# Performance work log

Measured on AMD Instinct MI355X. Metric: run time of the kernel, lower is better.

## Reference

```python
import jax, jax.numpy as jnp
import numpy as np
from jax.scipy.special import logsumexp

B, F, V, C, K, KP = 8192, 32, 64, 32, 8, 7  # batch, features, values/feature, classes, gate options, padded pair candidates
TEMP = 1.0
EPS = 1e-06


def _structure():
    # candidate 0 = self table; candidates 1..7 = pair tables conditioned on preceding features
    mask = np.zeros((F - 1, K), dtype=bool)
    mask[:, 0] = True
    cond = np.zeros((F - 1, KP), dtype=np.int32)
    for i in range(F - 1):
        fi = i + 1
        for j in range(min(fi, KP)):
            mask[i, j + 1] = True
            cond[i, j] = fi - 1 - j
    return jnp.asarray(cond), jnp.asarray(mask)


def setup_inputs() -> dict:
    key = jax.random.key(0)
    ks = jax.random.split(key, 6)
    cond_index, valid_mask = _structure()
    return {
        "x": jax.random.randint(ks[0], (B, F), 0, V, dtype=jnp.int32),
        "training": True,
        "class_logits": jax.random.normal(ks[1], (C,), jnp.float32) * 0.1,
        "table0": jax.random.normal(ks[2], (V, C), jnp.float32) * 0.1,
        "self_tables": jax.random.normal(ks[3], (F - 1, V, C), jnp.float32) * 0.1,
        "pair_tables": jax.random.normal(ks[4], (F - 1, KP, V, V, C), jnp.float32) * 0.1,
        "structure_logits": jax.random.normal(ks[5], (F - 1, K), jnp.float32) * 0.1,
        "u_noise": jax.random.uniform(jax.random.fold_in(key, 7), (F - 1, K), jnp.float32),
        "cond_index": cond_index,
        "valid_mask": valid_mask,
    }


def reference(x, training, class_logits, table0, self_tables, pair_tables,
              structure_logits, u_noise, cond_index, valid_mask):
    # class prior term
    cl = class_logits - logsumexp(class_logits)  # [C]
    t0 = table0 - logsumexp(table0, axis=0, keepdims=True)  # [V,C]
    out = cl[None, :] + t0[x[:, 0]]  # [B,C]

    # Gumbel-softmax gate over candidate parent sets (training path)
    g = -jnp.log(-jnp.log(u_noise + EPS) + EPS)
    gate_logits = jnp.where(valid_mask, (structure_logits + g) / TEMP, -jnp.inf)
    w = jax.nn.softmax(gate_logits, axis=-1)  # [F-1,K]; padded entries get weight 0

    f_idx = jnp.arange(F - 1)
    xs = x[:, 1:]  # [B,F-1] feature values

    # self (class-only) candidate tables, normalized over the feature-value axis
    st = self_tables - logsumexp(self_tables, axis=1, keepdims=True)  # [F-1,V,C]
    self_g = st[f_idx[None, :], xs]  # [B,F-1,C]
    out = out + jnp.einsum('bfc,f->bc', self_g, w[:, 0])

    # pair candidate tables, normalized over the feature-value axis (axis 2)
    pt = pair_tables - logsumexp(pair_tables, axis=2, keepdims=True)  # [F-1,KP,V,V,C]
    xc = x[:, cond_index]  # [B,F-1,KP] conditioning feature values
    k_idx = jnp.arange(KP)
    pair_g = pt[f_idx[None, :, None], k_idx[None, None, :], xs[:, :, None], xc]  # [B,F-1,KP,C]
    out = out + jnp.einsum('bfkc,fk->bc', pair_g, w[:, 1:])
    return out
```

## Files before the change

kernel.cpp:

```cpp
#include <hip/hip_runtime.h>
#include <math.h>

#define B_  8192
#define F_  32
#define V_  64
#define C_  32
#define KP_ 7
#define EPS_ 1e-6f

#define WS_G 512

__global__ __launch_bounds__(1024)
void prep_kernel(const float* __restrict__ cl, const float* __restrict__ t0,
                 const float* __restrict__ st, const float* __restrict__ sl,
                 const float* __restrict__ un, float* __restrict__ ws) {
    __shared__ float gl[31][8];
    __shared__ float wsm[31][8];
    __shared__ float lse_self[31][32];
    int tid = threadIdx.x;

    if (tid < 248) {
        int f = tid >> 3, k = tid & 7;
        int kmax = min(f + 1, KP_);
        bool valid = (k <= kmax);
        float u = un[tid];
        float g = -__logf(-__logf(u + EPS_) + EPS_);
        gl[f][k] = valid ? (sl[tid] + g) : -INFINITY;
    }
    __syncthreads();
    if (tid < 248) {
        int f = tid >> 3, k = tid & 7;
        float m = -INFINITY;
        #pragma unroll
        for (int j = 0; j < 8; j++) m = fmaxf(m, gl[f][j]);
        float s = 0.f;
        #pragma unroll
        for (int j = 0; j < 8; j++) s += __expf(gl[f][j] - m);
        float wv = __expf(gl[f][k] - m) / s;
        wsm[f][k] = wv;
        ws[tid] = wv;
    }
    if (tid < 992) {
        int f = tid >> 5, c = tid & 31;
        float s = 0.f;
        #pragma unroll 8
        for (int v = 0; v < V_; v++) s += __expf(st[(f * V_ + v) * C_ + c]);
        lse_self[f][c] = __logf(s);
    }
    __syncthreads();
    if (tid < 32) {
        int c = tid;
        float scl = 0.f;
        #pragma unroll
        for (int j = 0; j < C_; j++) scl += __expf(cl[j]);
        float lse_cl = __logf(scl);
        float s0 = 0.f;
        #pragma unroll 8
        for (int v = 0; v < V_; v++) s0 += __expf(t0[v * C_ + c]);
        float lse_t0 = __logf(s0);
        float acc = cl[c] - lse_cl - lse_t0;
        for (int f = 0; f < 31; f++) acc -= wsm[f][0] * lse_self[f][c];
        ws[256 + c] = acc;
    }
}

__global__ __launch_bounds__(256)
void build_g_kernel(const float* __restrict__ t0, const float* __restrict__ st,
                    const float* __restrict__ pt, const float* __restrict__ ws,
                    float* __restrict__ G) {
    int idx = blockIdx.x * 256 + threadIdx.x;
    int c = idx & 31, v = (idx >> 5) & 63, j = idx >> 11;
    int nk = min(KP_, 31 - j);
    const float* bp[KP_];
    #pragma unroll
    for (int k = 0; k < KP_; k++) {
        int f = j + k;
        int fk = f * KP_ + k;
        bp[k] = pt + (fk * (V_ * V_) + v) * C_ + c;
    }
    float s[KP_];
    #pragma unroll
    for (int k = 0; k < KP_; k++) s[k] = 0.f;
    for (int a = 0; a < V_; a += 2) {
        float l0[KP_], l1[KP_];
        #pragma unroll
        for (int k = 0; k < KP_; k++) if (k < nk) {
            l0[k] = bp[k][a * (V_ * C_)];
            l1[k] = bp[k][(a + 1) * (V_ * C_)];
        }
        #pragma unroll
        for (int k = 0; k < KP_; k++) if (k < nk) {
            s[k] += __expf(l0[k]);
            s[k] += __expf(l1[k]);
        }
    }
    float g = 0.f;
    #pragma unroll
    for (int k = 0; k < KP_; k++) if (k < nk)
        g -= ws[(j + k) * 8 + k + 1] * __logf(s[k]);
    if (j == 0) g += t0[v * C_ + c];
    else        g += ws[(j - 1) * 8] * st[((j - 1) * V_ + v) * C_ + c];
    G[idx] = g;
}

__global__ __launch_bounds__(256)
void main_kernel(const int* __restrict__ x, const float* __restrict__ pt,
                 const float* __restrict__ ws, float* __restrict__ out) {
    __shared__ int   xsh[256];
    __shared__ float wsh[248];
    __shared__ float offsh[32];
    int tid = threadIdx.x;
    int fchunk = blockIdx.x >> 10;
    int bblk   = blockIdx.x & 1023;
    xsh[tid] = x[bblk * 256 + tid];
    if (tid < 248) wsh[tid] = ws[tid];
    if (tid < 32)  offsh[tid] = ws[256 + tid];
    __syncthreads();

    const float* __restrict__ G = ws + WS_G;
    int c = tid & 31;
    int r = tid >> 5;
    const int* xrow = &xsh[r * 32];
    float acc = 0.f;

    if (fchunk == 0) {
        acc = offsh[c];
        #pragma unroll
        for (int j = 0; j < 16; j++)
            acc += G[(j * V_ + xrow[j]) * C_ + c];
        for (int f = 0; f < 6; f++) {
            int xv = xrow[f + 1];
            const float* bp = pt + ((f * KP_) * V_ + xv) * (V_ * C_) + c;
            float pv[6];
            for (int k = 0; k <= f; k++)
                pv[k] = bp[k * (V_ * V_ * C_) + xrow[f - k] * C_];
            for (int k = 0; k <= f; k++)
                acc += wsh[f * 8 + k + 1] * pv[k];
        }
        #pragma unroll 2
        for (int f = 6; f < 17; f++) {
            int xv = xrow[f + 1];
            const float* bp = pt + ((f * KP_) * V_ + xv) * (V_ * C_) + c;
            float pv[KP_];
            #pragma unroll
            for (int k = 0; k < KP_; k++)
                pv[k] = bp[k * (V_ * V_ * C_) + xrow[f - k] * C_];
            #pragma unroll
            for (int k = 0; k < KP_; k++)
                acc += wsh[f * 8 + k + 1] * pv[k];
        }
    } else {
        #pragma unroll
        for (int j = 16; j < 32; j++)
            acc += G[(j * V_ + xrow[j]) * C_ + c];
        #pragma unroll 2
        for (int f = 17; f < 31; f++) {
            int xv = xrow[f + 1];
            const float* bp = pt + ((f * KP_) * V_ + xv) * (V_ * C_) + c;
            float pv[KP_];
            #pragma unroll
            for (int k = 0; k < KP_; k++)
                pv[k] = bp[k * (V_ * V_ * C_) + xrow[f - k] * C_];
            #pragma unroll
            for (int k = 0; k < KP_; k++)
                acc += wsh[f * 8 + k + 1] * pv[k];
        }
    }
    atomicAdd(&out[bblk * 256 + tid], acc);
}

extern "C" void kernel_launch(void* const* d_in, const int* in_sizes, int n_in,
                              void* d_out, int out_size, void* d_ws, size_t ws_size,
                              hipStream_t stream) {
    const int*   x   = (const int*)  d_in[0];
    const float* cl  = (const float*)d_in[2];
    const float* t0  = (const float*)d_in[3];
    const float* st  = (const float*)d_in[4];
    const float* pt  = (const float*)d_in[5];
    const float* sl  = (const float*)d_in[6];
    const float* un  = (const float*)d_in[7];
    float* ws  = (float*)d_ws;
    float* out = (float*)d_out;

    hipMemsetAsync(out, 0, (size_t)B_ * C_ * sizeof(float), stream);
    prep_kernel<<<1, 1024, 0, stream>>>(cl, t0, st, sl, un, ws);
    build_g_kernel<<<256, 256, 0, stream>>>(t0, st, pt, ws, ws + WS_G);
    main_kernel<<<2048, 256, 0, stream>>>(x, pt, ws, out);
}
```

Measured before the change: 233.5 us.

## Split features across warps within a block and reduce in shared memory instead of atomics

Each block now covers two batch rows instead of eight. Its four 64-thread groups each take a balanced slice of the G-table lookups and pair-table gathers, roughly 49 pair gathers per group. Partial sums are combined through shared memory and written once with a plain store. This removes the output memset and the global atomicAdds, and doubles the number of blocks to give more parallelism. In exchange it adds a block-wide barrier and leaves three quarters of the threads idle during the final store.

```diff
diff --git a/kernel.cpp b/kernel.cpp
--- a/kernel.cpp
+++ b/kernel.cpp
@@ -106,28 +106,31 @@
 __global__ __launch_bounds__(256)
 void main_kernel(const int* __restrict__ x, const float* __restrict__ pt,
                  const float* __restrict__ ws, float* __restrict__ out) {
-    __shared__ int   xsh[256];
+    __shared__ int   xsh[64];
     __shared__ float wsh[248];
     __shared__ float offsh[32];
+    __shared__ float part[3][64];
     int tid = threadIdx.x;
-    int fchunk = blockIdx.x >> 10;
-    int bblk   = blockIdx.x & 1023;
-    xsh[tid] = x[bblk * 256 + tid];
+    if (tid < 64)  xsh[tid] = x[blockIdx.x * 64 + tid];
     if (tid < 248) wsh[tid] = ws[tid];
     if (tid < 32)  offsh[tid] = ws[256 + tid];
     __syncthreads();
 
     const float* __restrict__ G = ws + WS_G;
+    int q = tid >> 6;
+    int r = (tid >> 5) & 1;
     int c = tid & 31;
-    int r = tid >> 5;
     const int* xrow = &xsh[r * 32];
     float acc = 0.f;
 
-    if (fchunk == 0) {
-        acc = offsh[c];
-        #pragma unroll
-        for (int j = 0; j < 16; j++)
-            acc += G[(j * V_ + xrow[j]) * C_ + c];
+    #pragma unroll
+    for (int jj = 0; jj < 8; jj++) {
+        int j = q * 8 + jj;
+        acc += G[(j * V_ + xrow[j]) * C_ + c];
+    }
+
+    if (q == 0) {
+        acc += offsh[c];
         for (int f = 0; f < 6; f++) {
             int xv = xrow[f + 1];
             const float* bp = pt + ((f * KP_) * V_ + xv) * (V_ * C_) + c;
@@ -138,7 +141,7 @@
                 acc += wsh[f * 8 + k + 1] * pv[k];
         }
         #pragma unroll 2
-        for (int f = 6; f < 17; f++) {
+        for (int f = 6; f < 10; f++) {
             int xv = xrow[f + 1];
             const float* bp = pt + ((f * KP_) * V_ + xv) * (V_ * C_) + c;
             float pv[KP_];
@@ -150,11 +153,10 @@
                 acc += wsh[f * 8 + k + 1] * pv[k];
         }
     } else {
-        #pragma unroll
-        for (int j = 16; j < 32; j++)
-            acc += G[(j * V_ + xrow[j]) * C_ + c];
+        int fbeg = 10 + (q - 1) * 7;
         #pragma unroll 2
-        for (int f = 17; f < 31; f++) {
+        for (int ff = 0; ff < 7; ff++) {
+            int f = fbeg + ff;
             int xv = xrow[f + 1];
             const float* bp = pt + ((f * KP_) * V_ + xv) * (V_ * C_) + c;
             float pv[KP_];
@@ -166,7 +168,13 @@
                 acc += wsh[f * 8 + k + 1] * pv[k];
         }
     }
-    atomicAdd(&out[bblk * 256 + tid], acc);
+
+    if (q > 0) part[q - 1][r * 32 + c] = acc;
+    __syncthreads();
+    if (q == 0) {
+        acc += part[0][tid] + part[1][tid] + part[2][tid];
+        out[blockIdx.x * 64 + tid] = acc;
+    }
 }
 
 extern "C" void kernel_launch(void* const* d_in, const int* in_sizes, int n_in,
@@ -182,8 +190,7 @@
     float* ws  = (float*)d_ws;
     float* out = (float*)d_out;
 
-    hipMemsetAsync(out, 0, (size_t)B_ * C_ * sizeof(float), stream);
     prep_kernel<<<1, 1024, 0, stream>>>(cl, t0, st, sl, un, ws);
     build_g_kernel<<<256, 256, 0, stream>>>(t0, st, pt, ws, ws + WS_G);
-    main_kernel<<<2048, 256, 0, stream>>>(x, pt, ws, out);
+    main_kernel<<<4096, 256, 0, stream>>>(x, pt, ws, out);
 }
```

Measured after the change: 231.1 us. Within noise of the previous version (-1.1%).
